# Performance work log

Measured on AMD Instinct MI355X. Metric: run time of the kernel, lower is better.

Reference implementation:

```python
import jax, jax.numpy as jnp
import numpy as np

STRIDE = (1, 1)
PADDING = (1, 1)
DILATION = (1, 1)


def deform_conv(x, offset, weight, stride=STRIDE, padding=PADDING, dilation=DILATION):
    """Deformable convolution v1 (mmcv layout), deformable_groups=1, groups=1.

    x:      [B, C, H, W]
    offset: [B, 2*kh*kw, Ho, Wo]   pairs ordered (dy, dx) per kernel tap
    weight: [Co, C, kh, kw]
    """
    B, C, H, W = x.shape
    Co, Ci, kh, kw = weight.shape
    sh, sw = stride
    ph, pw = padding
    dh, dw = dilation
    Ho = (H + 2 * ph - (dh * (kh - 1) + 1)) // sh + 1
    Wo = (W + 2 * pw - (dw * (kw - 1) + 1)) // sw + 1
    K2 = kh * kw

    off = offset.reshape(B, K2, 2, Ho, Wo)
    # base sampling grid per kernel tap: [K2, Ho, Wo]
    ky = (jnp.arange(K2) // kw) * dh          # kernel row offsets
    kx = (jnp.arange(K2) % kw) * dw           # kernel col offsets
    hi = jnp.arange(Ho) * sh - ph             # output-row -> input-row base
    wi = jnp.arange(Wo) * sw - pw
    py = off[:, :, 0] + (ky[:, None, None] + hi[None, :, None])  # [B,K2,Ho,Wo]
    px = off[:, :, 1] + (kx[:, None, None] + wi[None, None, :])  # [B,K2,Ho,Wo]

    y0 = jnp.floor(py)
    x0 = jnp.floor(px)
    ly = py - y0
    lx = px - x0
    hy = 1.0 - ly
    hx = 1.0 - lx
    y0i = y0.astype(jnp.int32)
    x0i = x0.astype(jnp.int32)
    y1i = y0i + 1
    x1i = x0i + 1

    xf = x.reshape(B, C, H * W)

    def gather(yi, xi):
        # zero padding outside the image, per-corner validity (DCN semantics)
        valid = (yi >= 0) & (yi < H) & (xi >= 0) & (xi < W)
        yc = jnp.clip(yi, 0, H - 1)
        xc = jnp.clip(xi, 0, W - 1)
        idx = (yc * W + xc).reshape(B, -1)                 # [B, K2*Ho*Wo]
        vals = jax.vmap(lambda xb, ib: xb[:, ib])(xf, idx)  # [B, C, K2*Ho*Wo]
        vals = vals.reshape(B, C, K2, Ho, Wo)
        return vals * valid[:, None].astype(x.dtype)

    # im2col with bilinear sampling: [B, C, K2, Ho, Wo]
    col = (gather(y0i, x0i) * (hy * hx)[:, None]
           + gather(y0i, x1i) * (hy * lx)[:, None]
           + gather(y1i, x0i) * (ly * hx)[:, None]
           + gather(y1i, x1i) * (ly * lx)[:, None])

    # GEMM: out[b,o,h,w] = sum_{c,k} W[o,c,k] * col[b,c,k,h,w]
    out = jnp.einsum('bckhw,ock->bohw', col, weight.reshape(Co, Ci, K2))
    return out


def setup_inputs() -> dict:
    key = jax.random.key(0)
    k1, k2, k3 = jax.random.split(key, 3)
    x = jax.random.normal(k1, (4, 256, 64, 64), dtype=jnp.float32)
    offset = jax.random.normal(k2, (4, 18, 64, 64), dtype=jnp.float32)
    n = 256 * 3 * 3
    stdv = 1.0 / np.sqrt(n)
    weight = jax.random.uniform(k3, (256, 256, 3, 3), dtype=jnp.float32,
                                minval=-stdv, maxval=stdv)
    return {"x": x, "offset": offset, "weight": weight}


def reference(x, offset, weight):
    return deform_conv(x, offset, weight)
```

## Files before the change

### kernel.cpp

```cpp
#include <hip/hip_runtime.h>
#include <hip/hip_bf16.h>
#include <cstddef>

#define B_    4
#define C_    256
#define H_    64
#define W_    64
#define CO_   256
#define K2_   9
#define NSTEP 72

typedef __attribute__((ext_vector_type(8))) short short8;
typedef __attribute__((ext_vector_type(4))) float f32x4;

__device__ __forceinline__ unsigned short f2bf(float f) {
    unsigned u = __builtin_bit_cast(unsigned, f);
    u = (u + 0x7fffu + ((u >> 16) & 1u)) >> 16;
    return (unsigned short)u;
}
__device__ __forceinline__ unsigned pack2bf(float lo, float hi) {
    __hip_bfloat162 h = __float22bfloat162_rn(make_float2(lo, hi));
    unsigned r; __builtin_memcpy(&r, &h, 4);
    return r;
}
__device__ __forceinline__ float bflo(unsigned u) {
    return __builtin_bit_cast(float, u << 16);
}
__device__ __forceinline__ float bfhi(unsigned u) {
    return __builtin_bit_cast(float, u & 0xffff0000u);
}

__global__ void wpack_kernel(const float* __restrict__ w,
                             unsigned short* __restrict__ wpk) {
    const int idx = blockIdx.x * 256 + threadIdx.x;
    if (idx >= NSTEP * 16 * 64) return;
    const int lane = idx & 63;
    const int mt   = (idx >> 6) & 15;
    const int s    = idx >> 10;
    const int o    = mt * 16 + (lane & 15);
    const int cc   = s / 9;
    const int t    = s - 9 * cc;
    const int c0   = cc * 32 + ((lane >> 4) << 3);
    unsigned short h[8];
#pragma unroll
    for (int e = 0; e < 8; ++e)
        h[e] = f2bf(w[(o * C_ + c0 + e) * K2_ + t]);
    uint4 v;
    v.x = h[0] | ((unsigned)h[1] << 16);
    v.y = h[2] | ((unsigned)h[3] << 16);
    v.z = h[4] | ((unsigned)h[5] << 16);
    v.w = h[6] | ((unsigned)h[7] << 16);
    *reinterpret_cast<uint4*>(&wpk[(size_t)idx * 8]) = v;
}

__device__ __forceinline__ short8 loadA(const unsigned short* __restrict__ wpk,
                                        const float* __restrict__ wraw,
                                        int use_pk, int s, int mt, int lane) {
    if (use_pk) {
        return *reinterpret_cast<const short8*>(
            wpk + (((size_t)(s * 16 + mt) * 64 + lane) << 3));
    } else {
        const int cc = s / 9;
        const int t  = s - 9 * cc;
        const int c0 = cc * 32 + ((lane >> 4) << 3);
        const int o  = mt * 16 + (lane & 15);
        short8 r;
#pragma unroll
        for (int e = 0; e < 8; ++e)
            r[e] = (short)f2bf(wraw[(o * C_ + c0 + e) * K2_ + t]);
        return r;
    }
}

__global__ __launch_bounds__(512, 4)
void dcn_mfma_kernel(const float* __restrict__ x,
                     const float* __restrict__ off,
                     const unsigned short* __restrict__ wpk,
                     const float* __restrict__ wraw,
                     float* __restrict__ out,
                     int use_pk) {
    __shared__ __align__(16) unsigned s_win[32 * 484];
    __shared__ unsigned s_mw01[K2_ * 32];
    __shared__ unsigned s_mw23[K2_ * 32];
    __shared__ int      s_menc[K2_ * 32];
    __shared__ __align__(16) unsigned short s_colb[2][3][1024];

    const int tid = threadIdx.x;
    const int bid = blockIdx.x;
    const int xcd  = bid & 7;
    const int slot = bid >> 3;
    const int b    = xcd >> 1;
    const int ho   = ((xcd & 1) << 5) | (slot >> 1);
    const int woh  = slot & 1;
    const int wo0  = woh << 5;

    const char* xb8 = (const char*)x + ((size_t)b << 22);

    if (tid < K2_ * 32) {
        const int t = tid >> 5;
        const int p = tid & 31;
        const int pa = wo0 + p;
        const float dy = off[((b * 18 + 2 * t    ) * 64 + ho) * 64 + pa];
        const float dx = off[((b * 18 + 2 * t + 1) * 64 + ho) * 64 + pa];
        const float py = (float)(ho - 1 + t / 3) + dy;
        const float px = (float)(pa - 1 + t % 3) + dx;
        const float y0f = floorf(py), x0f = floorf(px);
        const float ly = py - y0f, lx = px - x0f;
        const float hy = 1.0f - ly, hx = 1.0f - lx;
        const int y0 = (int)y0f, x0 = (int)x0f;
        const int y1 = y0 + 1,   x1 = x0 + 1;
        const bool vy0 = (y0 >= 0) & (y0 < H_);
        const bool vy1 = (y1 >= 0) & (y1 < H_);
        const bool vx0 = (x0 >= 0) & (x0 < W_);
        const bool vx1 = (x1 >= 0) & (x1 < W_);
        const int yc0 = min(max(y0, 0), H_ - 1);
        const int yc1 = min(max(y1, 0), H_ - 1);
        const int xc0 = min(max(x0, 0), W_ - 1);
        const int xc1 = min(max(x1, 0), W_ - 1);
        float w00 = (vy0 && vx0) ? hy * hx : 0.0f;
        float w01 = (vy0 && vx1) ? hy * lx : 0.0f;
        float w10 = (vy1 && vx0) ? ly * hx : 0.0f;
        float w11 = (vy1 && vx1) ? ly * lx : 0.0f;
        const int dys = yc1 - yc0, dxs = xc1 - xc0;
        if (!dxs) { w00 += w01; w01 = 0.0f; w10 += w11; w11 = 0.0f; }
        if (!dys) { w00 += w10; w10 = 0.0f; w01 += w11; w11 = 0.0f; }
        const int r0 = yc0 - (ho - 5);
        const int j0 = xc0 - (wo0 - 8);
        const bool fast = (r0 >= 0) & (r0 + dys <= 10) & (j0 >= 0) & (j0 <= 43);
        int enc;
        if (fast)
            enc = ((r0 * 44 + j0) << 2) | dys;
        else
            enc = (int)(0x80000000u
                        | (unsigned)((((yc0 << 6) + xc0) << 2) | (dys << 1) | dxs));
        s_mw01[t * 32 + p] = pack2bf(w00, w01);
        s_mw23[t * 32 + p] = pack2bf(w10, w11);
        s_menc[t * 32 + p] = enc;
    }

    unsigned stoff[8];
#pragma unroll
    for (int v = 0; v < 8; ++v) {
        const int u = tid + (v << 9);
        if (u < 3872) {
            const int cl  = u / 121;
            const int rem = u - cl * 121;
            const int r   = rem / 11;
            const int q   = rem - r * 11;
            const int y   = ho - 5 + r;
            int gof = (((y << 6) + wo0 - 8) << 2) + (q << 4);
            gof = min(max(gof, 0), 16368);
            if ((unsigned)y >= 64u) gof = 0;
            stoff[v] = ((unsigned)cl << 14) + (unsigned)gof;
        } else {
            stoff[v] = 0xffffffffu;
        }
    }

    const int lane = tid & 63;
    const int wave = tid >> 6;
    const int wo   = lane & 31;
    const int kk0  = (wave << 2) | ((lane >> 5) << 1);
    const unsigned swr = ((unsigned)(wo >> 4) << 10)
                       | ((unsigned)((wo & 15) | ((kk0 >> 3) << 4)) << 4)
                       | ((unsigned)(kk0 & 7) << 1);
    const int mt0  = (wave >> 1) << 2;
    const unsigned brd = ((unsigned)(wave & 1) << 10) | ((unsigned)lane << 4);
    const char* winC = (const char*)s_win + kk0 * 1936;

    f32x4 acc[4];
#pragma unroll
    for (int m = 0; m < 4; ++m) acc[m] = (f32x4)(0.0f);

#define STAGEW(XCB_) do {                                                      \
        char* wb_ = (char*)s_win + (size_t)tid * 16;                           \
        _Pragma("unroll")                                                      \
        for (int v_ = 0; v_ < 8; ++v_) {                                       \
            const unsigned so_ = stoff[v_];                                    \
            if (so_ != 0xffffffffu) {                                          \
                const float4 g_ = *(const float4*)((XCB_) + so_);              \
                const unsigned in_ = so_ & 16383u;                             \
                const float g4_ = *(const float*)((XCB_)                       \
                                    + (in_ >= 16368u ? so_ : so_ + 16));       \
                uint4 pk_;                                                     \
                pk_.x = pack2bf(g_.x, g_.y);                                   \
                pk_.y = pack2bf(g_.y, g_.z);                                   \
                pk_.z = pack2bf(g_.z, g_.w);                                   \
                pk_.w = pack2bf(g_.w, g4_);                                    \
                *(uint4*)(wb_ + v_ * 8192) = pk_;                              \
            }                                                                  \
        }                                                                      \
    } while (0)

#define COLT1(T_, BUFB_, JJ_, XCB_) do {                                       \
        const unsigned u01_ = s_mw01[(T_) * 32 + wo];                          \
        const unsigned u23_ = s_mw23[(T_) * 32 + wo];                          \
        const int mb_ = s_menc[(T_) * 32 + wo];                                \
        const float w0_ = bflo(u01_), w1_ = bfhi(u01_);                        \
        const float w2_ = bflo(u23_), w3_ = bfhi(u23_);                        \
        float vA_, vB_;                                                        \
        if (__builtin_expect(mb_ >= 0, 1)) {                                   \
            const char* pA_ = winC + (mb_ & ~3);                               \
            const int dr_ = (mb_ & 1) ? 176 : 0;                               \
            const unsigned a0_ = *(const unsigned*)(pA_);                      \
            const unsigned a1_ = *(const unsigned*)(pA_ + dr_);                \
            const unsigned c0_ = *(const unsigned*)(pA_ + 1936);               \
            const unsigned c1_ = *(const unsigned*)(pA_ + 1936 + dr_);         \
            vA_ = w0_*bflo(a0_) + w1_*bfhi(a0_) + w2_*bflo(a1_) + w3_*bfhi(a1_); \
            vB_ = w0_*bflo(c0_) + w1_*bfhi(c0_) + w2_*bflo(c1_) + w3_*bfhi(c1_); \
        } else {                                                               \
            const int dxb_ = (mb_ & 1) << 2, dyb_ = (mb_ & 2) << 7;            \
            const int o_ = mb_ & 0x3fffc;                                      \
            const char* plA_ = (XCB_) + ((size_t)kk0 << 14);                   \
            const char* plB_ = plA_ + (1 << 14);                               \
            vA_ = w0_ * *(const float*)(plA_ + o_)                             \
                + w1_ * *(const float*)(plA_ + o_ + dxb_)                      \
                + w2_ * *(const float*)(plA_ + o_ + dyb_)                      \
                + w3_ * *(const float*)(plA_ + o_ + dyb_ + dxb_);              \
            vB_ = w0_ * *(const float*)(plB_ + o_)                             \
                + w1_ * *(const float*)(plB_ + o_ + dxb_)                      \
                + w2_ * *(const float*)(plB_ + o_ + dyb_)                      \
                + w3_ * *(const float*)(plB_ + o_ + dyb_ + dxb_);              \
        }                                                                      \
        *(unsigned*)((char*)(BUFB_) + (JJ_) * 2048 + swr) = pack2bf(vA_, vB_); \
    } while (0)

#define COL3(T0_, BUFB_, XCB_) do {                                            \
        COLT1((T0_),     BUFB_, 0, XCB_);                                      \
        COLT1((T0_) + 1, BUFB_, 1, XCB_);                                      \
        COLT1((T0_) + 2, BUFB_, 2, XCB_);                                      \
    } while (0)

#define MFMA_(A_, B_, C_) __builtin_amdgcn_mfma_f32_16x16x32_bf16(A_, B_, C_, 0, 0, 0)

#define GEMM3(S0_, BUFB_) do {                                                 \
        _Pragma("unroll")                                                      \
        for (int js_ = 0; js_ < 3; ++js_) {                                    \
            const short8 a0_ = loadA(wpk, wraw, use_pk, (S0_) + js_, mt0,     lane); \
            const short8 a1_ = loadA(wpk, wraw, use_pk, (S0_) + js_, mt0 + 1, lane); \
            const short8 a2_ = loadA(wpk, wraw, use_pk, (S0_) + js_, mt0 + 2, lane); \
            const short8 a3_ = loadA(wpk, wraw, use_pk, (S0_) + js_, mt0 + 3, lane); \
            const short8 bb_ = *(const short8*)((const char*)(BUFB_)           \
                                                + js_ * 2048 + brd);           \
            acc[0] = MFMA_(a0_, bb_, acc[0]);                                  \
            acc[1] = MFMA_(a1_, bb_, acc[1]);                                  \
            acc[2] = MFMA_(a2_, bb_, acc[2]);                                  \
            acc[3] = MFMA_(a3_, bb_, acc[3]);                                  \
        }                                                                      \
    } while (0)

#define BARLG() do {                                                           \
        asm volatile("s_waitcnt lgkmcnt(0)" ::: "memory");                     \
        __builtin_amdgcn_s_barrier();                                          \
    } while (0)

    STAGEW(xb8);
    __syncthreads();
    COL3(0, (char*)s_colb, xb8);
    BARLG();

    for (int cc = 0; cc < 8; ++cc) {
        const char* xcb  = xb8 + ((size_t)cc << 19);
        const char* xcbN = xb8 + ((size_t)(cc + 1) << 19);
        const int p = cc & 1;
        char* bufP = (char*)s_colb + p * 6144;
        char* bufQ = (char*)s_colb + (p ^ 1) * 6144;
        const int s0 = cc * 9;

        COL3(3, bufQ, xcb);
        GEMM3(s0, bufP);
        BARLG();

        COL3(6, bufP, xcb);
        GEMM3(s0 + 3, bufQ);
        BARLG();

        if (cc < 7) STAGEW(xcbN);
        GEMM3(s0 + 6, bufP);
        BARLG();

        if (cc < 7) {
            COL3(0, bufQ, xcbN);
            BARLG();
        }
    }

#undef STAGEW
#undef COLT1
#undef COL3
#undef MFMA_
#undef GEMM3
#undef BARLG

    const int ncol = wo0 + ((wave & 1) << 4) + (lane & 15);
#pragma unroll
    for (int m = 0; m < 4; ++m) {
        const int ob = (mt0 + m) * 16 + ((lane >> 4) << 2);
#pragma unroll
        for (int r = 0; r < 4; ++r) {
            out[(((size_t)(b * CO_ + ob + r) * 64 + ho) << 6) + ncol] = acc[m][r];
        }
    }
}

extern "C" void kernel_launch(void* const* d_in, const int* in_sizes, int n_in,
                              void* d_out, int out_size, void* d_ws, size_t ws_size,
                              hipStream_t stream) {
    const float* x      = (const float*)d_in[0];
    const float* offset = (const float*)d_in[1];
    const float* weight = (const float*)d_in[2];
    float* out = (float*)d_out;

    const size_t pk_bytes = (size_t)NSTEP * 16 * 64 * 8 * 2;
    const int use_pk = (ws_size >= pk_bytes) ? 1 : 0;
    unsigned short* wpk = (unsigned short*)d_ws;

    if (use_pk) {
        wpack_kernel<<<288, 256, 0, stream>>>(weight, wpk);
    }
    dcn_mfma_kernel<<<512, 512, 0, stream>>>(x, offset, wpk, weight, out, use_pk);
}
```

Before: 79.76 us.

## Restructure DCN pipeline to per-tap double buffering with register-prefetched weights

Replaces the three-tap column batches and triple-buffered LDS with a per-tap two-buffer ping-pong loop, where each step prefetches the next step's weight fragments into registers before building the next column tile and issuing MFMAs. The bilinear interpolation in the fast path now uses bf16 dot2 instructions on packed weights and samples, and the two weight arrays are interleaved into one. Staging the next channel chunk is no longer overlapped with a GEMM step and needs an extra full barrier. This triples the number of barriers per chunk and shrinks the work between barriers, which may expose more latency.

```diff
diff --git a/kernel.cpp b/kernel.cpp
--- a/kernel.cpp
+++ b/kernel.cpp
@@ -28,6 +28,22 @@
 }
 __device__ __forceinline__ float bfhi(unsigned u) {
     return __builtin_bit_cast(float, u & 0xffff0000u);
+}
+
+#if defined(__has_builtin)
+#if __has_builtin(__builtin_amdgcn_fdot2_f32_bf16)
+#define HAS_BFDOT2 1
+#endif
+#endif
+__device__ __forceinline__ float dot2bf(unsigned x, unsigned w, float acc) {
+#ifdef HAS_BFDOT2
+    typedef __attribute__((ext_vector_type(2))) __bf16 bf16x2;
+    return __builtin_amdgcn_fdot2_f32_bf16(__builtin_bit_cast(bf16x2, x),
+                                           __builtin_bit_cast(bf16x2, w),
+                                           acc, false);
+#else
+    return acc + bflo(x) * bflo(w) + bfhi(x) * bfhi(w);
+#endif
 }
 
 __global__ void wpack_kernel(const float* __restrict__ w,
@@ -80,10 +96,9 @@
                      float* __restrict__ out,
                      int use_pk) {
     __shared__ __align__(16) unsigned s_win[32 * 484];
-    __shared__ unsigned s_mw01[K2_ * 32];
-    __shared__ unsigned s_mw23[K2_ * 32];
-    __shared__ int      s_menc[K2_ * 32];
-    __shared__ __align__(16) unsigned short s_colb[2][3][1024];
+    __shared__ __align__(8)  unsigned s_mwp[K2_ * 32 * 2];
+    __shared__ int s_menc[K2_ * 32];
+    __shared__ __align__(16) unsigned short s_colb[2][1024];
 
     const int tid = threadIdx.x;
     const int bid = blockIdx.x;
@@ -133,8 +148,8 @@
         else
             enc = (int)(0x80000000u
                         | (unsigned)((((yc0 << 6) + xc0) << 2) | (dys << 1) | dxs));
-        s_mw01[t * 32 + p] = pack2bf(w00, w01);
-        s_mw23[t * 32 + p] = pack2bf(w10, w11);
+        s_mwp[(t * 32 + p) * 2    ] = pack2bf(w00, w01);
+        s_mwp[(t * 32 + p) * 2 + 1] = pack2bf(w10, w11);
         s_menc[t * 32 + p] = enc;
     }
 
@@ -192,12 +207,11 @@
         }                                                                      \
     } while (0)
 
-#define COLT1(T_, BUFB_, JJ_, XCB_) do {                                       \
-        const unsigned u01_ = s_mw01[(T_) * 32 + wo];                          \
-        const unsigned u23_ = s_mw23[(T_) * 32 + wo];                          \
+#define COLT1(T_, BUFB_, XCB_) do {                                            \
+        const unsigned* mp_ = &s_mwp[((T_) * 32 + wo) * 2];                    \
+        const unsigned u01_ = mp_[0];                                          \
+        const unsigned u23_ = mp_[1];                                          \
         const int mb_ = s_menc[(T_) * 32 + wo];                                \
-        const float w0_ = bflo(u01_), w1_ = bfhi(u01_);                        \
-        const float w2_ = bflo(u23_), w3_ = bfhi(u23_);                        \
         float vA_, vB_;                                                        \
         if (__builtin_expect(mb_ >= 0, 1)) {                                   \
             const char* pA_ = winC + (mb_ & ~3);                               \
@@ -206,9 +220,11 @@
             const unsigned a1_ = *(const unsigned*)(pA_ + dr_);                \
             const unsigned c0_ = *(const unsigned*)(pA_ + 1936);               \
             const unsigned c1_ = *(const unsigned*)(pA_ + 1936 + dr_);         \
-            vA_ = w0_*bflo(a0_) + w1_*bfhi(a0_) + w2_*bflo(a1_) + w3_*bfhi(a1_); \
-            vB_ = w0_*bflo(c0_) + w1_*bfhi(c0_) + w2_*bflo(c1_) + w3_*bfhi(c1_); \
+            vA_ = dot2bf(a1_, u23_, dot2bf(a0_, u01_, 0.0f));                  \
+            vB_ = dot2bf(c1_, u23_, dot2bf(c0_, u01_, 0.0f));                  \
         } else {                                                               \
+            const float w0_ = bflo(u01_), w1_ = bfhi(u01_);                    \
+            const float w2_ = bflo(u23_), w3_ = bfhi(u23_);                    \
             const int dxb_ = (mb_ & 1) << 2, dyb_ = (mb_ & 2) << 7;            \
             const int o_ = mb_ & 0x3fffc;                                      \
             const char* plA_ = (XCB_) + ((size_t)kk0 << 14);                   \
@@ -222,31 +238,17 @@
                 + w2_ * *(const float*)(plB_ + o_ + dyb_)                      \
                 + w3_ * *(const float*)(plB_ + o_ + dyb_ + dxb_);              \
         }                                                                      \
-        *(unsigned*)((char*)(BUFB_) + (JJ_) * 2048 + swr) = pack2bf(vA_, vB_); \
+        *(unsigned*)((char*)(BUFB_) + swr) = pack2bf(vA_, vB_);                \
     } while (0)
 
-#define COL3(T0_, BUFB_, XCB_) do {                                            \
-        COLT1((T0_),     BUFB_, 0, XCB_);                                      \
-        COLT1((T0_) + 1, BUFB_, 1, XCB_);                                      \
-        COLT1((T0_) + 2, BUFB_, 2, XCB_);                                      \
-    } while (0)
-
 #define MFMA_(A_, B_, C_) __builtin_amdgcn_mfma_f32_16x16x32_bf16(A_, B_, C_, 0, 0, 0)
 
-#define GEMM3(S0_, BUFB_) do {                                                 \
-        _Pragma("unroll")                                                      \
-        for (int js_ = 0; js_ < 3; ++js_) {                                    \
-            const short8 a0_ = loadA(wpk, wraw, use_pk, (S0_) + js_, mt0,     lane); \
-            const short8 a1_ = loadA(wpk, wraw, use_pk, (S0_) + js_, mt0 + 1, lane); \
-            const short8 a2_ = loadA(wpk, wraw, use_pk, (S0_) + js_, mt0 + 2, lane); \
-            const short8 a3_ = loadA(wpk, wraw, use_pk, (S0_) + js_, mt0 + 3, lane); \
-            const short8 bb_ = *(const short8*)((const char*)(BUFB_)           \
-                                                + js_ * 2048 + brd);           \
-            acc[0] = MFMA_(a0_, bb_, acc[0]);                                  \
-            acc[1] = MFMA_(a1_, bb_, acc[1]);                                  \
-            acc[2] = MFMA_(a2_, bb_, acc[2]);                                  \
-            acc[3] = MFMA_(a3_, bb_, acc[3]);                                  \
-        }                                                                      \
+#define GEMM4(BUFB_) do {                                                      \
+        const short8 bb_ = *(const short8*)((const char*)(BUFB_) + brd);       \
+        acc[0] = MFMA_(aC0, bb_, acc[0]);                                      \
+        acc[1] = MFMA_(aC1, bb_, acc[1]);                                      \
+        acc[2] = MFMA_(aC2, bb_, acc[2]);                                      \
+        acc[3] = MFMA_(aC3, bb_, acc[3]);                                      \
     } while (0)
 
 #define BARLG() do {                                                           \
@@ -254,42 +256,54 @@
         __builtin_amdgcn_s_barrier();                                          \
     } while (0)
 
+    char* const buf0 = (char*)s_colb;
+    char* const buf1 = (char*)s_colb + 2048;
+
     STAGEW(xb8);
     __syncthreads();
-    COL3(0, (char*)s_colb, xb8);
+    COLT1(0, buf0, xb8);
+    short8 aC0 = loadA(wpk, wraw, use_pk, 0, mt0,     lane);
+    short8 aC1 = loadA(wpk, wraw, use_pk, 0, mt0 + 1, lane);
+    short8 aC2 = loadA(wpk, wraw, use_pk, 0, mt0 + 2, lane);
+    short8 aC3 = loadA(wpk, wraw, use_pk, 0, mt0 + 3, lane);
     BARLG();
 
     for (int cc = 0; cc < 8; ++cc) {
         const char* xcb  = xb8 + ((size_t)cc << 19);
         const char* xcbN = xb8 + ((size_t)(cc + 1) << 19);
-        const int p = cc & 1;
-        char* bufP = (char*)s_colb + p * 6144;
-        char* bufQ = (char*)s_colb + (p ^ 1) * 6144;
-        const int s0 = cc * 9;
-
-        COL3(3, bufQ, xcb);
-        GEMM3(s0, bufP);
-        BARLG();
-
-        COL3(6, bufP, xcb);
-        GEMM3(s0 + 3, bufQ);
-        BARLG();
-
-        if (cc < 7) STAGEW(xcbN);
-        GEMM3(s0 + 6, bufP);
-        BARLG();
+
+        for (int j = 0; j < 9; ++j) {
+            const int s = cc * 9 + j;
+            short8 aN0, aN1, aN2, aN3;
+            const bool pf = (s + 1 < NSTEP);
+            if (pf) {
+                aN0 = loadA(wpk, wraw, use_pk, s + 1, mt0,     lane);
+                aN1 = loadA(wpk, wraw, use_pk, s + 1, mt0 + 1, lane);
+                aN2 = loadA(wpk, wraw, use_pk, s + 1, mt0 + 2, lane);
+                aN3 = loadA(wpk, wraw, use_pk, s + 1, mt0 + 3, lane);
+            }
+            if (j < 8) {
+                if (j & 1) COLT1(j + 1, buf0, xcb);
+                else       COLT1(j + 1, buf1, xcb);
+            }
+            if (j & 1) GEMM4(buf1);
+            else       GEMM4(buf0);
+            BARLG();
+            if (pf) { aC0 = aN0; aC1 = aN1; aC2 = aN2; aC3 = aN3; }
+        }
 
         if (cc < 7) {
-            COL3(0, bufQ, xcbN);
+            STAGEW(xcbN);
+            __syncthreads();
+            COLT1(0, buf0, xcbN);
             BARLG();
         }
     }
 
 #undef STAGEW
 #undef COLT1
-#undef COL3
 #undef MFMA_
-#undef GEMM3
+#undef GEMM4
 #undef BARLG
 
     const int ncol = wo0 + ((wave & 1) << 4) + (lane & 15);
```

Measured after the change: 104.5 us. 31.1% more time.
